# Kernel optimization log

Hardware: AMD Instinct MI355X
Metric: run time of the kernel (lower is better)

Reference implementation:

```python
import jax, jax.numpy as jnp
import numpy as np

B, T = 64, 1000
RNN_DIM, EMB_DIM, ATT_DIM, LOC_DIM, KSIZE = 1024, 512, 128, 32, 31


def setup_inputs() -> dict:
    key = jax.random.key(0)
    ks = jax.random.split(key, 8)
    s = 0.02  # small init scale for weights
    return {
        "attention_hidden_state": jax.random.normal(ks[0], (B, RNN_DIM), jnp.float32),
        "memory": jax.random.normal(ks[1], (B, T, EMB_DIM), jnp.float32),
        "processed_memory": jax.random.normal(ks[2], (B, T, ATT_DIM), jnp.float32),
        "attention_weights_cat": jax.random.uniform(ks[3], (B, 2, T), jnp.float32),
        "mask": jnp.zeros((B, T), dtype=bool),
        "W_query": jax.random.normal(ks[4], (ATT_DIM, RNN_DIM), jnp.float32) * s,
        "conv_w": jax.random.normal(ks[5], (LOC_DIM, 2, KSIZE), jnp.float32) * s,
        "W_loc": jax.random.normal(ks[6], (ATT_DIM, LOC_DIM), jnp.float32) * s,
        "v": jax.random.normal(ks[7], (1, ATT_DIM), jnp.float32) * s,
    }


def reference(attention_hidden_state, memory, processed_memory,
              attention_weights_cat, mask, W_query, conv_w, W_loc, v):
    # processed_query: (B, 1, ATT_DIM)
    pq = (attention_hidden_state @ W_query.T)[:, None, :]
    # location features: conv1d over (B, 2, T), SAME padding, no bias
    loc = jax.lax.conv_general_dilated(
        attention_weights_cat, conv_w,
        window_strides=(1,), padding="SAME",
        dimension_numbers=("NCH", "OIH", "NCH"))  # (B, LOC_DIM, T)
    loc = jnp.einsum("bct,ac->bta", loc, W_loc)  # (B, T, ATT_DIM)
    # energies: v . tanh(pq + loc + processed_memory) -> (B, T)
    energy = jnp.einsum("bta,oa->bt", jnp.tanh(pq + loc + processed_memory), v)
    energy = jnp.where(mask, -jnp.inf, energy)
    attention_weights = jax.nn.softmax(energy, axis=1)  # (B, T)
    attention_context = jnp.einsum("bt,bte->be", attention_weights, memory)
    return attention_context, attention_weights
```

## Files before the change

kernel.cpp:

```cpp
#include <hip/hip_runtime.h>
#include <hip/hip_bf16.h>
#include <math.h>

#define B 64
#define T 1000
#define RNN_DIM 1024
#define EMB_DIM 512
#define ATT_DIM 128
#define LOC_DIM 32
#define KSIZE 31
#define PAD 15
#define ET 64
#define CHUNK 50

__global__ __launch_bounds__(256) void pq_kernel(
    const float* __restrict__ hidden,
    const float* __restrict__ Wq,
    float* __restrict__ pq)
{
    int gwave = (blockIdx.x * blockDim.x + threadIdx.x) >> 6;
    int lane  = threadIdx.x & 63;
    int b = gwave >> 7;
    int a = gwave & 127;

    const float4* h4 = (const float4*)(hidden + (size_t)b * RNN_DIM);
    const float4* w4 = (const float4*)(Wq + (size_t)a * RNN_DIM);

    float acc = 0.f;
#pragma unroll
    for (int j = 0; j < 4; ++j) {
        float4 h = h4[j * 64 + lane];
        float4 w = w4[j * 64 + lane];
        acc += h.x * w.x + h.y * w.y + h.z * w.z + h.w * w.w;
    }
#pragma unroll
    for (int off = 32; off > 0; off >>= 1)
        acc += __shfl_down(acc, off, 64);
    if (lane == 0) pq[gwave] = acc;
}

__global__ __launch_bounds__(256) void energy_kernel(
    const float* __restrict__ aw,
    const float* __restrict__ cw,
    const float* __restrict__ wl,
    const float* __restrict__ pq,
    const float* __restrict__ pm,
    const float* __restrict__ v,
    float* __restrict__ energy)
{
    __shared__ float aw_lds[2][ET + 2 * PAD];
    __shared__ float cw_lds[LOC_DIM][2][KSIZE];
    __shared__ float wl_lds[ATT_DIM][36];
    __shared__ float pq_lds[ATT_DIM];
    __shared__ float v_lds[ATT_DIM];
    __shared__ float loc_lds[ET][36];
    __shared__ float pm_lds[ET][132];

    const int b   = blockIdx.x;
    const int t0  = blockIdx.y * ET;
    const int tid = threadIdx.x;

    const float4* pm4 = (const float4*)(pm + (size_t)b * T * ATT_DIM);
    for (int i = tid; i < ET * 32; i += 256) {
        int t = i >> 5, c4 = i & 31;
        int tt = t0 + t;
        float4 val = make_float4(0.f, 0.f, 0.f, 0.f);
        if (tt < T) val = pm4[(size_t)tt * 32 + c4];
        *((float4*)&pm_lds[t][c4 * 4]) = val;
    }
    for (int i = tid; i < LOC_DIM * 2 * KSIZE; i += 256)
        ((float*)cw_lds)[i] = cw[i];
    for (int i = tid; i < ATT_DIM * LOC_DIM; i += 256)
        wl_lds[i >> 5][i & 31] = wl[i];
    if (tid < ATT_DIM) {
        pq_lds[tid] = pq[b * ATT_DIM + tid];
        v_lds[tid]  = v[tid];
    }
    for (int i = tid; i < 2 * (ET + 2 * PAD); i += 256) {
        int ch = i / (ET + 2 * PAD);
        int p  = i % (ET + 2 * PAD);
        int t  = t0 + p - PAD;
        aw_lds[ch][p] = (t >= 0 && t < T) ? aw[(size_t)b * 2 * T + ch * T + t] : 0.f;
    }
    __syncthreads();

    {
        const int c  = tid & 31;
        const int tg = tid >> 5;
        float acc[8];
#pragma unroll
        for (int j = 0; j < 8; ++j) acc[j] = 0.f;
#pragma unroll
        for (int ch = 0; ch < 2; ++ch) {
            float awr[KSIZE + 7];
#pragma unroll
            for (int j = 0; j < KSIZE + 7; ++j) awr[j] = aw_lds[ch][tg * 8 + j];
#pragma unroll
            for (int k = 0; k < KSIZE; ++k) {
                float cv = cw_lds[c][ch][k];
#pragma unroll
                for (int j = 0; j < 8; ++j) acc[j] += cv * awr[k + j];
            }
        }
#pragma unroll
        for (int j = 0; j < 8; ++j) loc_lds[tg * 8 + j][c] = acc[j];
    }
    __syncthreads();

    {
        const int tl = tid >> 2;
        const int aq = tid & 3;

        float lr[32];
#pragma unroll
        for (int j = 0; j < 8; ++j)
            *((float4*)&lr[4 * j]) = *((const float4*)&loc_lds[tl][4 * j]);

        float acc = 0.f;
#pragma unroll 4
        for (int aa = 0; aa < 32; ++aa) {
            const int a = aq + 4 * aa;
            float e = pq_lds[a] + pm_lds[tl][a];
#pragma unroll
            for (int j = 0; j < 8; ++j) {
                float4 w4 = *((const float4*)&wl_lds[a][4 * j]);
                e += w4.x * lr[4*j] + w4.y * lr[4*j+1] + w4.z * lr[4*j+2] + w4.w * lr[4*j+3];
            }
            float ex = __expf(2.f * e);
            float th = 1.f - 2.f * __builtin_amdgcn_rcpf(1.f + ex);
            acc += v_lds[a] * th;
        }
        acc += __shfl_xor(acc, 1, 64);
        acc += __shfl_xor(acc, 2, 64);
        if (aq == 0 && (t0 + tl) < T)
            energy[b * T + t0 + tl] = acc;
    }
}

__global__ __launch_bounds__(256) void softmax_kernel(
    const float* __restrict__ energy,
    const unsigned char* __restrict__ mask,
    float* __restrict__ out)
{
    int b   = blockIdx.x;
    int tid = threadIdx.x;

    for (int i = tid; i < EMB_DIM; i += 256) out[b * EMB_DIM + i] = 0.f;

    __shared__ float red[4];
    float e[4];
    float mx = -INFINITY;
#pragma unroll
    for (int j = 0; j < 4; ++j) {
        int t = tid + j * 256;
        if (t < T) {
            float val = energy[b * T + t];
            if (mask[b * T + t]) val = -INFINITY;
            e[j] = val;
            mx = fmaxf(mx, val);
        } else e[j] = -INFINITY;
    }
#pragma unroll
    for (int off = 32; off > 0; off >>= 1)
        mx = fmaxf(mx, __shfl_down(mx, off, 64));
    if ((tid & 63) == 0) red[tid >> 6] = mx;
    __syncthreads();
    mx = fmaxf(fmaxf(red[0], red[1]), fmaxf(red[2], red[3]));
    __syncthreads();

    float sum = 0.f;
    float ex[4];
#pragma unroll
    for (int j = 0; j < 4; ++j) {
        ex[j] = (e[j] == -INFINITY) ? 0.f : expf(e[j] - mx);
        sum += ex[j];
    }
#pragma unroll
    for (int off = 32; off > 0; off >>= 1)
        sum += __shfl_down(sum, off, 64);
    if ((tid & 63) == 0) red[tid >> 6] = sum;
    __syncthreads();
    sum = red[0] + red[1] + red[2] + red[3];
    float inv = 1.f / sum;
#pragma unroll
    for (int j = 0; j < 4; ++j) {
        int t = tid + j * 256;
        if (t < T) out[B * EMB_DIM + b * T + t] = ex[j] * inv;
    }
}

__global__ __launch_bounds__(256) void context_kernel(
    const float* __restrict__ memory,
    const float* __restrict__ w,
    float* __restrict__ ctx)
{
    int b  = blockIdx.x;
    int t0 = blockIdx.y * CHUNK;
    int e4 = threadIdx.x & 127;
    int ts = threadIdx.x >> 7;

    const float4* mem4 = (const float4*)(memory + (size_t)b * T * EMB_DIM);
    float4 acc = {0.f, 0.f, 0.f, 0.f};
    for (int t = t0 + ts; t < t0 + CHUNK; t += 2) {
        float wt = w[b * T + t];
        float4 m = mem4[(size_t)t * 128 + e4];
        acc.x += wt * m.x; acc.y += wt * m.y;
        acc.z += wt * m.z; acc.w += wt * m.w;
    }
    float* dst = ctx + b * EMB_DIM + e4 * 4;
    atomicAdd(dst + 0, acc.x);
    atomicAdd(dst + 1, acc.y);
    atomicAdd(dst + 2, acc.z);
    atomicAdd(dst + 3, acc.w);
}

extern "C" void kernel_launch(void* const* d_in, const int* in_sizes, int n_in,
                              void* d_out, int out_size, void* d_ws, size_t ws_size,
                              hipStream_t stream) {
    const float* hidden = (const float*)d_in[0];
    const float* memory = (const float*)d_in[1];
    const float* pm     = (const float*)d_in[2];
    const float* aw     = (const float*)d_in[3];
    const unsigned char* mask = (const unsigned char*)d_in[4];
    const float* Wq     = (const float*)d_in[5];
    const float* cw     = (const float*)d_in[6];
    const float* wl     = (const float*)d_in[7];
    const float* v      = (const float*)d_in[8];

    float* out = (float*)d_out;

    float* pq_ws     = (float*)d_ws;
    float* energy_ws = pq_ws + B * ATT_DIM;

    pq_kernel<<<dim3((B * ATT_DIM) / 4), dim3(256), 0, stream>>>(hidden, Wq, pq_ws);

    energy_kernel<<<dim3(B, (T + ET - 1) / ET), dim3(256), 0, stream>>>(
        aw, cw, wl, pq_ws, pm, v, energy_ws);

    softmax_kernel<<<dim3(B), dim3(256), 0, stream>>>(energy_ws, mask, out);

    context_kernel<<<dim3(B, T / CHUNK), dim3(256), 0, stream>>>(
        memory, out + B * EMB_DIM, out);
}
```

Baseline: 281.4 us.

## Replace atomic context reduction with partial sums plus a second reduction kernel

The context reduction now splits T into 50 chunks of 20 steps per batch, writes per-chunk partial vectors to workspace, and sums them in a separate kernel instead of using float atomics. Each block stages its weights in shared memory, runs two independent accumulators, and reduces across waves in LDS. This removes the atomic traffic and the zero-init in softmax and raises grid parallelism, at the cost of an extra launch and a round trip of the partials through memory.

```diff
diff --git a/kernel.cpp b/kernel.cpp
--- a/kernel.cpp
+++ b/kernel.cpp
@@ -11,7 +11,8 @@
 #define KSIZE 31
 #define PAD 15
 #define ET 64
-#define CHUNK 50
+#define CCH 20
+#define NCH (T / CCH)
 
 __global__ __launch_bounds__(256) void pq_kernel(
     const float* __restrict__ hidden,
@@ -145,8 +146,6 @@
     int b   = blockIdx.x;
     int tid = threadIdx.x;
 
-    for (int i = tid; i < EMB_DIM; i += 256) out[b * EMB_DIM + i] = 0.f;
-
     __shared__ float red[4];
     float e[4];
     float mx = -INFINITY;
@@ -189,29 +188,74 @@
     }
 }
 
-__global__ __launch_bounds__(256) void context_kernel(
+__global__ __launch_bounds__(256) void context_part_kernel(
     const float* __restrict__ memory,
     const float* __restrict__ w,
+    float* __restrict__ part)
+{
+    __shared__ float w_lds[CCH];
+    __shared__ float4 red[4][64];
+
+    const int b    = blockIdx.x;
+    const int c    = blockIdx.y;
+    const int t0   = c * CCH;
+    const int tid  = threadIdx.x;
+    const int lane = tid & 63;
+    const int wv   = tid >> 6;
+    const int h    = wv & 1;
+    const int tp   = wv >> 1;
+
+    if (tid < CCH) w_lds[tid] = w[b * T + t0 + tid];
+    __syncthreads();
+
+    const float4* mem4 = (const float4*)(memory + (size_t)b * T * EMB_DIM);
+    float4 a0 = {0.f, 0.f, 0.f, 0.f};
+    float4 a1 = {0.f, 0.f, 0.f, 0.f};
+#pragma unroll
+    for (int i = 0; i < CCH / 4; ++i) {
+        int ta = t0 + tp + 4 * i;
+        int tb = ta + 2;
+        float wa = w_lds[tp + 4 * i];
+        float wb = w_lds[tp + 4 * i + 2];
+        float4 ma = mem4[(size_t)ta * 128 + h * 64 + lane];
+        float4 mb = mem4[(size_t)tb * 128 + h * 64 + lane];
+        a0.x += wa * ma.x; a0.y += wa * ma.y; a0.z += wa * ma.z; a0.w += wa * ma.w;
+        a1.x += wb * mb.x; a1.y += wb * mb.y; a1.z += wb * mb.z; a1.w += wb * mb.w;
+    }
+    a0.x += a1.x; a0.y += a1.y; a0.z += a1.z; a0.w += a1.w;
+
+    red[wv][lane] = a0;
+    __syncthreads();
+    if (tid < 128) {
+        int hh = tid >> 6, e4 = tid & 63;
+        float4 s0 = red[hh][e4];
+        float4 s1 = red[hh + 2][e4];
+        float4 s;
+        s.x = s0.x + s1.x; s.y = s0.y + s1.y;
+        s.z = s0.z + s1.z; s.w = s0.w + s1.w;
+        float4* p4 = (float4*)(part + ((size_t)b * NCH + c) * EMB_DIM);
+        p4[hh * 64 + e4] = s;
+    }
+}
+
+__global__ __launch_bounds__(256) void context_sum_kernel(
+    const float* __restrict__ part,
     float* __restrict__ ctx)
 {
-    int b  = blockIdx.x;
-    int t0 = blockIdx.y * CHUNK;
-    int e4 = threadIdx.x & 127;
-    int ts = threadIdx.x >> 7;
-
-    const float4* mem4 = (const float4*)(memory + (size_t)b * T * EMB_DIM);
-    float4 acc = {0.f, 0.f, 0.f, 0.f};
-    for (int t = t0 + ts; t < t0 + CHUNK; t += 2) {
-        float wt = w[b * T + t];
-        float4 m = mem4[(size_t)t * 128 + e4];
-        acc.x += wt * m.x; acc.y += wt * m.y;
-        acc.z += wt * m.z; acc.w += wt * m.w;
-    }
-    float* dst = ctx + b * EMB_DIM + e4 * 4;
-    atomicAdd(dst + 0, acc.x);
-    atomicAdd(dst + 1, acc.y);
-    atomicAdd(dst + 2, acc.z);
-    atomicAdd(dst + 3, acc.w);
+    const int b = blockIdx.x;
+    const int e = blockIdx.y * 256 + threadIdx.x;
+    const float* p = part + (size_t)b * NCH * EMB_DIM + e;
+    float s0 = 0.f, s1 = 0.f, s2 = 0.f, s3 = 0.f;
+#pragma unroll
+    for (int c = 0; c < NCH - 2; c += 4) {
+        s0 += p[(c + 0) * EMB_DIM];
+        s1 += p[(c + 1) * EMB_DIM];
+        s2 += p[(c + 2) * EMB_DIM];
+        s3 += p[(c + 3) * EMB_DIM];
+    }
+    s0 += p[(NCH - 2) * EMB_DIM];
+    s1 += p[(NCH - 1) * EMB_DIM];
+    ctx[b * EMB_DIM + e] = (s0 + s1) + (s2 + s3);
 }
 
 extern "C" void kernel_launch(void* const* d_in, const int* in_sizes, int n_in,
@@ -231,6 +275,7 @@
 
     float* pq_ws     = (float*)d_ws;
     float* energy_ws = pq_ws + B * ATT_DIM;
+    float* part_ws   = energy_ws + B * T;
 
     pq_kernel<<<dim3((B * ATT_DIM) / 4), dim3(256), 0, stream>>>(hidden, Wq, pq_ws);
 
@@ -239,6 +284,8 @@
 
     softmax_kernel<<<dim3(B), dim3(256), 0, stream>>>(energy_ws, mask, out);
 
-    context_kernel<<<dim3(B, T / CHUNK), dim3(256), 0, stream>>>(
-        memory, out + B * EMB_DIM, out);
-}
+    context_part_kernel<<<dim3(B, NCH), dim3(256), 0, stream>>>(
+        memory, out + B * EMB_DIM, part_ws);
+
+    context_sum_kernel<<<dim3(B, 2), dim3(256), 0, stream>>>(part_ws, out);
+}
```

New measurement: 268.5 us. 1.05x faster.
